# Kernel tuning notes

Measured on AMD Instinct MI355X. Metric: run time of the kernel, lower is better.

Reference implementation:

```python
import jax, jax.numpy as jnp
import numpy as np

EMBEDDING_DIM = 1024


def setup_inputs() -> dict:
    key = jax.random.key(0)
    x = jax.random.normal(key, (8, 4096, EMBEDDING_DIM), dtype=jnp.float32)
    return {"x": x}


def reference(x):
    # x: [B, S, D]. pe[pos, i] = sin(pos / 10000**((i//2)/S)) if i even else cos(...)
    # NOTE: faithful to source: exponent denominator is len_sequence S, not D.
    S = x.shape[1]
    D = x.shape[2]
    pos = jnp.arange(S, dtype=jnp.float32)[:, None]            # [S, 1]
    i = jnp.arange(D)                                          # [D]
    k = (i // 2).astype(jnp.float32)[None, :]                  # [1, D]
    angle = pos / jnp.power(jnp.float32(10000.0), k / jnp.float32(S))  # [S, D]
    pe = jnp.where((i % 2 == 0)[None, :], jnp.sin(angle), jnp.cos(angle))
    return x + pe[None, :, :].astype(x.dtype)
```

## Files before the change

kernel.cpp:

```cpp
#include <hip/hip_runtime.h>
#include <hip/hip_bf16.h>


#define PE_B 8
#define PE_S 4096
#define PE_D 1024

__global__ __launch_bounds__(256) void PositionalEncoding_84095459656362_kernel(
    const float* __restrict__ x, float* __restrict__ out) {
    const int t  = blockIdx.x * blockDim.x + threadIdx.x;
    const int d4 = (t & (PE_D / 4 - 1)) << 2;
    const int s  = t >> 8;

    const float c  = -0.0032440703857f;
    const float k0 = (float)(d4 >> 1);
    const float a0 = (float)s * __builtin_exp2f(k0 * c);
    const float a1 = (float)s * __builtin_exp2f((k0 + 1.0f) * c);

    float4 pe;
    __sincosf(a0, &pe.x, &pe.y);
    __sincosf(a1, &pe.z, &pe.w);

    size_t off = (size_t)s * PE_D + d4;
    const size_t batch_stride = (size_t)PE_S * PE_D;
#pragma unroll
    for (int b = 0; b < PE_B; ++b) {
        const float4 v = *(const float4*)(x + off);
        float4 r;
        r.x = v.x + pe.x;
        r.y = v.y + pe.y;
        r.z = v.z + pe.z;
        r.w = v.w + pe.w;
        *(float4*)(out + off) = r;
        off += batch_stride;
    }
}

extern "C" void kernel_launch(void* const* d_in, const int* in_sizes, int n_in,
                              void* d_out, int out_size, void* d_ws, size_t ws_size,
                              hipStream_t stream) {
    const float* x = (const float*)d_in[0];
    float* out = (float*)d_out;
    const int threads = PE_S * PE_D / 4;
    PositionalEncoding_84095459656362_kernel<<<threads / 256, 256, 0, stream>>>(x, out);
}
```

Before: 242.4 us.

## Use one thread per float4 across all batches with nontemporal stores

Switches from each thread looping over all 8 batches, reusing its computed encoding, to one thread per float4 element of the full tensor, so there are 8x more threads and the sin/cos is recomputed per batch. The second angle is now derived by multiplying the first by a constant ratio instead of a second exp2, and outputs are written with nontemporal stores. The aim is more memory-level parallelism and less cache pollution for a bandwidth-bound streaming add, at the cost of redundant transcendental work and slightly different rounding in the odd-pair angle.

Measured after the change: 221.9 us. -8.5%, faster.

```diff
diff --git a/kernel.cpp b/kernel.cpp
--- a/kernel.cpp
+++ b/kernel.cpp
@@ -2,38 +2,35 @@
 #include <hip/hip_bf16.h>
 
 
-#define PE_B 8
 #define PE_S 4096
 #define PE_D 1024
+#define N4   (8 * PE_S * PE_D / 4)
+
+typedef float f32x4 __attribute__((ext_vector_type(4)));
 
 __global__ __launch_bounds__(256) void PositionalEncoding_84095459656362_kernel(
     const float* __restrict__ x, float* __restrict__ out) {
-    const int t  = blockIdx.x * blockDim.x + threadIdx.x;
-    const int d4 = (t & (PE_D / 4 - 1)) << 2;
-    const int s  = t >> 8;
+    const int i  = blockIdx.x * blockDim.x + threadIdx.x;
+    const int d4 = (i & (PE_D / 4 - 1)) << 2;
+    const int s  = (i >> 8) & (PE_S - 1);
 
-    const float c  = -0.0032440703857f;
-    const float k0 = (float)(d4 >> 1);
-    const float a0 = (float)s * __builtin_exp2f(k0 * c);
-    const float a1 = (float)s * __builtin_exp2f((k0 + 1.0f) * c);
+    const float c   = -0.0032440703857f;
+    const float r1  = 0.99775390625f;
+    const float e0  = __builtin_exp2f((float)(d4 >> 1) * c);
+    const float a0  = (float)s * e0;
+    const float a1  = a0 * r1;
 
-    float4 pe;
-    __sincosf(a0, &pe.x, &pe.y);
-    __sincosf(a1, &pe.z, &pe.w);
+    float s0, c0, s1, c1;
+    __sincosf(a0, &s0, &c0);
+    __sincosf(a1, &s1, &c1);
 
-    size_t off = (size_t)s * PE_D + d4;
-    const size_t batch_stride = (size_t)PE_S * PE_D;
-#pragma unroll
-    for (int b = 0; b < PE_B; ++b) {
-        const float4 v = *(const float4*)(x + off);
-        float4 r;
-        r.x = v.x + pe.x;
-        r.y = v.y + pe.y;
-        r.z = v.z + pe.z;
-        r.w = v.w + pe.w;
-        *(float4*)(out + off) = r;
-        off += batch_stride;
-    }
+    const f32x4 v = ((const f32x4*)x)[i];
+    f32x4 r;
+    r.x = v.x + s0;
+    r.y = v.y + c0;
+    r.z = v.z + s1;
+    r.w = v.w + c1;
+    __builtin_nontemporal_store(r, &((f32x4*)out)[i]);
 }
 
 extern "C" void kernel_launch(void* const* d_in, const int* in_sizes, int n_in,
@@ -41,6 +38,5 @@
                               hipStream_t stream) {
     const float* x = (const float*)d_in[0];
     float* out = (float*)d_out;
-    const int threads = PE_S * PE_D / 4;
-    PositionalEncoding_84095459656362_kernel<<<threads / 256, 256, 0, stream>>>(x, out);
+    PositionalEncoding_84095459656362_kernel<<<N4 / 256, 256, 0, stream>>>(x, out);
 }
```
